# Optimization experiments

Measured on AMD Instinct MI355X. Metric: run time of the kernel, lower is better.

## Reference

```python
import jax, jax.numpy as jnp
import numpy as np

N_NODES = 50000
N_EDGES = 800000
IN_SIZE = 128
HID = 128
OUT_SIZE = 64
N_LAYERS = 2
MAXK = 32


def setup_inputs() -> dict:
    key = jax.random.key(0)
    ks = jax.random.split(key, 8)
    s = 0.05  # small init scale, xavier-like
    return {
        "x": jax.random.normal(ks[0], (N_NODES, IN_SIZE), dtype=jnp.float32),
        "W_in": jax.random.normal(ks[1], (IN_SIZE, HID), dtype=jnp.float32) * s,
        "b_in": jnp.zeros((HID,), dtype=jnp.float32),
        "W_self": jax.random.normal(ks[2], (N_LAYERS, HID, HID), dtype=jnp.float32) * s,
        "W_neigh": jax.random.normal(ks[3], (N_LAYERS, HID, HID), dtype=jnp.float32) * s,
        "W_out": jax.random.normal(ks[4], (HID, OUT_SIZE), dtype=jnp.float32) * s,
        "b_out": jnp.zeros((OUT_SIZE,), dtype=jnp.float32),
        "edge_index": jax.random.randint(ks[5], (2, N_EDGES), 0, N_NODES, dtype=jnp.int32),
        "k": MAXK,
    }


def _maxk(x, k):
    # Keep top-k values per row, zero out the rest (MaxK nonlinearity).
    vals, idx = jax.lax.top_k(x, k)                     # [N, k]
    rows = jnp.arange(x.shape[0])[:, None]
    return jnp.zeros_like(x).at[rows, idx].set(vals)


def reference(x, W_in, b_in, W_self, W_neigh, W_out, b_out, edge_index, k):
    N = x.shape[0]
    src, dst = edge_index[0], edge_index[1]
    # Row sums of the (src->dst) adjacency = out-degree of src, per original code.
    deg = jax.ops.segment_sum(jnp.ones((src.shape[0],), dtype=x.dtype), src,
                              num_segments=N)[:, None]  # [N, 1]
    h = x @ W_in + b_in                                  # lin_in
    for i in range(W_self.shape[0]):
        hs = _maxk(h, k)                                 # MaxK sparsify [N, H]
        # adj @ hs : out[i] = sum over edges (i -> j) of hs[j]; then mean-normalize
        agg = jax.ops.segment_sum(hs[dst], src, num_segments=N) / (deg + 1e-6)
        h = hs @ W_self[i] + agg @ W_neigh[i]            # h_self + h_neigh
        # dropout (eval) and Identity norm are no-ops
    return h @ W_out + b_out                             # lin_out
```

## Files before the change

### kernel.cpp

```cpp
#include <hip/hip_runtime.h>

#define KDIM 128

typedef _Float16 f16x8 __attribute__((ext_vector_type(8)));
typedef _Float16 f16x4 __attribute__((ext_vector_type(4)));
typedef float f32x16 __attribute__((ext_vector_type(16)));

#define NRANGE 6250
#define ECHUNK 3200

__global__ void hist_kernel(const int* __restrict__ src, int* __restrict__ cnt, int E) {
    const int r = blockIdx.x & 7;
    const int chunk = blockIdx.x >> 3;
    const int lo = r * NRANGE, hi = lo + NRANGE;
    const int base = chunk * ECHUNK;
    const int end = min(base + ECHUNK, E);
    for (int i = base + threadIdx.x; i < end; i += 256) {
        int s = src[i];
        if (s >= lo && s < hi) atomicAdd(&cnt[s], 1);
    }
}

__global__ void scatter_kernel(const int* __restrict__ src, const int* __restrict__ dst,
                               int* cursor, int* __restrict__ col, int E) {
    const int r = blockIdx.x & 7;
    const int chunk = blockIdx.x >> 3;
    const int lo = r * NRANGE, hi = lo + NRANGE;
    const int base = chunk * ECHUNK;
    const int end = min(base + ECHUNK, E);
    for (int i = base + threadIdx.x; i < end; i += 256) {
        int s = src[i];
        if (s >= lo && s < hi) {
            int p = atomicAdd(&cursor[s], 1);
            col[p] = dst[i];
        }
    }
}

__global__ void scan1_kernel(const int* __restrict__ cnt, int* __restrict__ row_ptr,
                             int* __restrict__ bsum, int N) {
    __shared__ int ws[4];
    const int t = threadIdx.x;
    const int lane = t & 63, w = t >> 6;
    const int i = blockIdx.x * 256 + t;
    int v = (i < N) ? cnt[i] : 0;
    int x = v;
    #pragma unroll
    for (int off = 1; off < 64; off <<= 1) {
        int u = __shfl_up(x, off);
        if (lane >= off) x += u;
    }
    if (lane == 63) ws[w] = x;
    __syncthreads();
    int wexcl = 0;
    #pragma unroll
    for (int k = 0; k < 4; k++) wexcl += (k < w) ? ws[k] : 0;
    if (i < N) row_ptr[i] = wexcl + x - v;
    if (t == 255) bsum[blockIdx.x] = wexcl + x;
}

__global__ void scan2_kernel(int* __restrict__ bsum, int NB) {
    __shared__ int ws[4];
    const int t = threadIdx.x;
    const int lane = t & 63, w = t >> 6;
    int v = (t < NB) ? bsum[t] : 0;
    int x = v;
    #pragma unroll
    for (int off = 1; off < 64; off <<= 1) {
        int u = __shfl_up(x, off);
        if (lane >= off) x += u;
    }
    if (lane == 63) ws[w] = x;
    __syncthreads();
    int wexcl = 0;
    #pragma unroll
    for (int k = 0; k < 4; k++) wexcl += (k < w) ? ws[k] : 0;
    if (t < NB) bsum[t] = wexcl + x - v;
}

__global__ void scan3_kernel(const int* __restrict__ bsum, int* __restrict__ row_ptr,
                             int* __restrict__ cursor, int N, int E) {
    const int i = blockIdx.x * 256 + threadIdx.x;
    if (i < N) {
        int v = row_ptr[i] + bsum[blockIdx.x];
        row_ptr[i] = v;
        cursor[i] = v;
    }
    if (i == 0) row_ptr[N] = E;
}

__global__ void sortrows_kernel(const int* __restrict__ row_ptr, int* __restrict__ col, int M) {
    int wid = (blockIdx.x * blockDim.x + threadIdx.x) >> 6;
    int lane = threadIdx.x & 63;
    if (wid >= M) return;
    int s = row_ptr[wid], e = row_ptr[wid + 1], len = e - s;
    if (len <= 1) return;
    if (len <= 64) {
        int v = (lane < len) ? col[s + lane] : 0x7fffffff;
        #pragma unroll
        for (int k = 2; k <= 64; k <<= 1) {
            #pragma unroll
            for (int j = k >> 1; j > 0; j >>= 1) {
                int o = __shfl_xor(v, j);
                bool dir = ((lane & k) == 0);
                bool smaller = ((lane & j) == 0);
                int mn = min(v, o), mx = max(v, o);
                v = (dir == smaller) ? mn : mx;
            }
        }
        if (lane < len) col[s + lane] = v;
    } else if (lane == 0) {
        for (int a = s + 1; a < e; a++) {
            int key = col[a];
            int b = a - 1;
            while (b >= s && col[b] > key) { col[b + 1] = col[b]; b--; }
            col[b + 1] = key;
        }
    }
}

__global__ void maxk_kernel(const float* __restrict__ h, float* __restrict__ hs, int M) {
    int wid = (blockIdx.x * blockDim.x + threadIdx.x) >> 6;
    int lane = threadIdx.x & 63;
    if (wid >= M) return;
    float2 v = ((const float2*)(h + (size_t)wid * KDIM))[lane];

    unsigned int u0 = __float_as_uint(v.x);
    u0 = (u0 & 0x80000000u) ? ~u0 : (u0 | 0x80000000u);
    unsigned int u1 = __float_as_uint(v.y);
    u1 = (u1 & 0x80000000u) ? ~u1 : (u1 | 0x80000000u);

    unsigned int prefix = 0;
    int remaining = 32;
    #pragma unroll
    for (int b = 31; b >= 0; --b) {
        unsigned int candHi = (prefix >> b) | 1u;
        unsigned long long m0 = __ballot((u0 >> b) == candHi);
        unsigned long long m1 = __ballot((u1 >> b) == candHi);
        int cnt = __popcll(m0) + __popcll(m1);
        if (cnt >= remaining) prefix |= (1u << b);
        else remaining -= cnt;
    }

    unsigned long long e0 = __ballot(u0 == prefix);
    unsigned long long e1 = __ballot(u1 == prefix);
    unsigned long long g0 = __ballot(u0 > prefix);
    unsigned long long g1 = __ballot(u1 > prefix);
    int quota = 32 - (__popcll(g0) + __popcll(g1));
    unsigned long long below = (1ULL << lane) - 1ULL;
    int rank0 = __popcll(e0 & below) + __popcll(e1 & below);
    int rank1 = rank0 + (int)((e0 >> lane) & 1ULL);
    bool k0 = (u0 > prefix) || (((e0 >> lane) & 1ULL) && rank0 < quota);
    bool k1 = (u1 > prefix) || (((e1 >> lane) & 1ULL) && rank1 < quota);

    float2 o;
    o.x = k0 ? v.x : 0.0f;
    o.y = k1 ? v.y : 0.0f;
    ((float2*)(hs + (size_t)wid * KDIM))[lane] = o;
}

__global__ __launch_bounds__(256)
void aggregate_kernel(const float* __restrict__ hs, const int* __restrict__ row_ptr,
                      const int* __restrict__ col, float* __restrict__ agg, int M) {
    const int lane = threadIdx.x & 63;
    const int wid = (blockIdx.x * blockDim.x + threadIdx.x) >> 6;
    if (wid >= M) return;
    const int s = row_ptr[wid], e = row_ptr[wid + 1];
    const float2* __restrict__ hp = (const float2*)hs;

    float2 a0 = make_float2(0.f, 0.f);
    float2 a1 = a0, a2 = a0, a3 = a0, a4 = a0, a5 = a0, a6 = a0, a7 = a0;

    int j = s;
    for (; j + 7 < e; j += 8) {
        int c0 = col[j];     int c1 = col[j + 1];
        int c2 = col[j + 2]; int c3 = col[j + 3];
        int c4 = col[j + 4]; int c5 = col[j + 5];
        int c6 = col[j + 6]; int c7 = col[j + 7];
        float2 v0 = hp[(size_t)c0 * 64 + lane];
        float2 v1 = hp[(size_t)c1 * 64 + lane];
        float2 v2 = hp[(size_t)c2 * 64 + lane];
        float2 v3 = hp[(size_t)c3 * 64 + lane];
        float2 v4 = hp[(size_t)c4 * 64 + lane];
        float2 v5 = hp[(size_t)c5 * 64 + lane];
        float2 v6 = hp[(size_t)c6 * 64 + lane];
        float2 v7 = hp[(size_t)c7 * 64 + lane];
        a0.x += v0.x; a0.y += v0.y;
        a1.x += v1.x; a1.y += v1.y;
        a2.x += v2.x; a2.y += v2.y;
        a3.x += v3.x; a3.y += v3.y;
        a4.x += v4.x; a4.y += v4.y;
        a5.x += v5.x; a5.y += v5.y;
        a6.x += v6.x; a6.y += v6.y;
        a7.x += v7.x; a7.y += v7.y;
    }
    if (j < e)     { float2 v = hp[(size_t)col[j]     * 64 + lane]; a0.x += v.x; a0.y += v.y; }
    if (j + 1 < e) { float2 v = hp[(size_t)col[j + 1] * 64 + lane]; a1.x += v.x; a1.y += v.y; }
    if (j + 2 < e) { float2 v = hp[(size_t)col[j + 2] * 64 + lane]; a2.x += v.x; a2.y += v.y; }
    if (j + 3 < e) { float2 v = hp[(size_t)col[j + 3] * 64 + lane]; a3.x += v.x; a3.y += v.y; }
    if (j + 4 < e) { float2 v = hp[(size_t)col[j + 4] * 64 + lane]; a4.x += v.x; a4.y += v.y; }
    if (j + 5 < e) { float2 v = hp[(size_t)col[j + 5] * 64 + lane]; a5.x += v.x; a5.y += v.y; }
    if (j + 6 < e) { float2 v = hp[(size_t)col[j + 6] * 64 + lane]; a6.x += v.x; a6.y += v.y; }

    float2 s01, s23, s45, s67, sA, sB, t;
    s01.x = a0.x + a1.x; s01.y = a0.y + a1.y;
    s23.x = a2.x + a3.x; s23.y = a2.y + a3.y;
    s45.x = a4.x + a5.x; s45.y = a4.y + a5.y;
    s67.x = a6.x + a7.x; s67.y = a6.y + a7.y;
    sA.x = s01.x + s23.x; sA.y = s01.y + s23.y;
    sB.x = s45.x + s67.x; sB.y = s45.y + s67.y;
    t.x = sA.x + sB.x; t.y = sA.y + sB.y;

    float inv = 1.0f / ((float)(e - s) + 1e-6f);
    float2 o;
    o.x = t.x * inv;
    o.y = t.y * inv;
    ((float2*)(agg + (size_t)wid * KDIM))[lane] = o;
}

__global__ void conv_wt_kernel(const float* __restrict__ W_in,
                               const float* __restrict__ W_self,
                               const float* __restrict__ W_neigh,
                               const float* __restrict__ W_out,
                               _Float16* __restrict__ wb) {
    int t = blockIdx.x * blockDim.x + threadIdx.x;
    if (t < 81920) {
        int m = t >> 14;
        int e = t & 16383;
        int n = e >> 7, k = e & 127;
        const float* S = (m == 0) ? W_in
                       : (m <= 2) ? (W_self + (size_t)(m - 1) * 16384)
                                  : (W_neigh + (size_t)(m - 3) * 16384);
        float v = S[k * 128 + n];
        _Float16 hi = (_Float16)v;
        _Float16 lo = (_Float16)(v - (float)hi);
        int pair = m * 2;
        wb[(size_t)pair * 16384 + n * 128 + k] = hi;
        wb[(size_t)(pair + 1) * 16384 + n * 128 + k] = lo;
    } else if (t < 90112) {
        int e = t - 81920;
        int n = e >> 7, k = e & 127;
        float v = W_out[k * 64 + n];
        _Float16 hi = (_Float16)v;
        _Float16 lo = (_Float16)(v - (float)hi);
        wb[(size_t)10 * 16384 + e] = hi;
        wb[(size_t)11 * 16384 + e] = lo;
    }
}

template <int BN, bool DUAL, bool BIAS>
__global__ __launch_bounds__(256)
void gemm_mfma(const float* __restrict__ A1, const float* __restrict__ A2,
               const _Float16* __restrict__ B1h, const _Float16* __restrict__ B1l,
               const _Float16* __restrict__ B2h, const _Float16* __restrict__ B2l,
               const float* __restrict__ bias, float* __restrict__ C, int M) {
    constexpr int NSRC = DUAL ? 2 : 1;
    constexpr int NT = BN / 32;
    constexpr int TPW = NT / 2;

    __shared__ __align__(16) char Alds[2 * 64 * 256];

    const int tid = threadIdx.x;
    const int w = tid >> 6;
    const int lane = tid & 63;
    const int l31 = lane & 31;
    const int kslot = lane >> 5;
    const int row0 = blockIdx.x * 64;

    const int n0 = (BN == 128) ? w * 32 : (w & 1) * 32;
    const int mt0 = (BN == 128) ? 0 : (w >> 1);

    f32x16 acc[TPW];
    #pragma unroll
    for (int t = 0; t < TPW; t++)
        #pragma unroll
        for (int e = 0; e < 16; e++) acc[t][e] = 0.0f;

    for (int s = 0; s < NSRC; s++) {
        if (s) __syncthreads();
        const float* A = s ? A2 : A1;
        #pragma unroll
        for (int p = 0; p < 8; p++) {
            int idx = tid + p * 256;
            int row = idx >> 5, k4 = idx & 31;
            float4 v = make_float4(0.f, 0.f, 0.f, 0.f);
            if (row0 + row < M) v = *(const float4*)(A + (size_t)(row0 + row) * KDIM + k4 * 4);
            _Float16 h0 = (_Float16)v.x, h1 = (_Float16)v.y,
                     h2 = (_Float16)v.z, h3 = (_Float16)v.w;
            f16x4 hv = {h0, h1, h2, h3};
            f16x4 lv = {(_Float16)(v.x - (float)h0), (_Float16)(v.y - (float)h1),
                        (_Float16)(v.z - (float)h2), (_Float16)(v.w - (float)h3)};
            int boff = (k4 * 8) ^ ((row & 7) << 4);
            *(f16x4*)(Alds + row * 256 + boff) = hv;
            *(f16x4*)(Alds + 16384 + row * 256 + boff) = lv;
        }
        __syncthreads();

        const _Float16* Bh = s ? B2h : B1h;
        const _Float16* Bl = s ? B2l : B1l;
        const _Float16* bph = Bh + (size_t)(n0 + l31) * 128 + kslot * 8;
        const _Float16* bpl = Bl + (size_t)(n0 + l31) * 128 + kslot * 8;
        #pragma unroll
        for (int kb = 0; kb < 8; kb++) {
            f16x8 bh = *(const f16x8*)(bph + kb * 16);
            f16x8 bl = *(const f16x8*)(bpl + kb * 16);
            #pragma unroll
            for (int t = 0; t < TPW; t++) {
                int row = (mt0 + t) * 32 + l31;
                int boff = ((kb * 2 + kslot) * 16) ^ ((row & 7) << 4);
                const char* rp = Alds + row * 256 + boff;
                f16x8 ah = *(const f16x8*)(rp);
                f16x8 al = *(const f16x8*)(rp + 16384);
                acc[t] = __builtin_amdgcn_mfma_f32_32x32x16_f16(al, bh, acc[t], 0, 0, 0);
                acc[t] = __builtin_amdgcn_mfma_f32_32x32x16_f16(ah, bl, acc[t], 0, 0, 0);
                acc[t] = __builtin_amdgcn_mfma_f32_32x32x16_f16(ah, bh, acc[t], 0, 0, 0);
            }
        }
    }

    float bv = 0.0f;
    if (BIAS) bv = bias[n0 + l31];
    #pragma unroll
    for (int t = 0; t < TPW; t++) {
        #pragma unroll
        for (int r = 0; r < 16; r++) {
            int row = row0 + (mt0 + t) * 32 + (r & 3) + 8 * (r >> 2) + 4 * kslot;
            if (row < M) C[(size_t)row * BN + n0 + l31] = acc[t][r] + bv;
        }
    }
}

extern "C" void kernel_launch(void* const* d_in, const int* in_sizes, int n_in,
                              void* d_out, int out_size, void* d_ws, size_t ws_size,
                              hipStream_t stream) {
    const float* x       = (const float*)d_in[0];
    const float* W_in    = (const float*)d_in[1];
    const float* b_in    = (const float*)d_in[2];
    const float* W_self  = (const float*)d_in[3];
    const float* W_neigh = (const float*)d_in[4];
    const float* W_out   = (const float*)d_in[5];
    const float* b_out   = (const float*)d_in[6];
    const int*   eidx    = (const int*)d_in[7];

    const int N = 50000, E = 800000;
    const int* src = eidx;
    const int* dst = eidx + E;

    char* ws = (char*)d_ws;
    float* h   = (float*)(ws);
    float* hs  = (float*)(ws + 25600000);
    float* agg = (float*)(ws + 51200000);
    int* cnt     = (int*)(ws + 76800000);
    int* row_ptr = (int*)(ws + 77000000);
    int* cursor  = (int*)(ws + 77200016);
    int* col     = (int*)(ws + 77400016);
    _Float16* wb = (_Float16*)(ws + 80600016);
    int* bsum    = (int*)(ws + 81000016);

    const _Float16* WinT_h  = wb + (size_t)0 * 16384;
    const _Float16* WinT_l  = wb + (size_t)1 * 16384;
    const _Float16* WoutT_h = wb + (size_t)10 * 16384;
    const _Float16* WoutT_l = wb + (size_t)11 * 16384;

    const int NB = (N + 255) / 256;
    const int EG = ((E + ECHUNK - 1) / ECHUNK) * 8;

    hipMemsetAsync(cnt, 0, N * sizeof(int), stream);
    hist_kernel<<<EG, 256, 0, stream>>>(src, cnt, E);
    scan1_kernel<<<NB, 256, 0, stream>>>(cnt, row_ptr, bsum, N);
    scan2_kernel<<<1, 256, 0, stream>>>(bsum, NB);
    scan3_kernel<<<NB, 256, 0, stream>>>(bsum, row_ptr, cursor, N, E);
    scatter_kernel<<<EG, 256, 0, stream>>>(src, dst, cursor, col, E);
    sortrows_kernel<<<(N + 3) / 4, 256, 0, stream>>>(row_ptr, col, N);
    conv_wt_kernel<<<(90112 + 255) / 256, 256, 0, stream>>>(W_in, W_self, W_neigh, W_out, wb);

    const int G = (N + 63) / 64;

    gemm_mfma<128, false, true><<<G, 256, 0, stream>>>(
        x, nullptr, WinT_h, WinT_l, nullptr, nullptr, b_in, h, N);

    for (int i = 0; i < 2; i++) {
        maxk_kernel<<<(N + 3) / 4, 256, 0, stream>>>(h, hs, N);
        aggregate_kernel<<<(N + 3) / 4, 256, 0, stream>>>(hs, row_ptr, col, agg, N);
        const _Float16* WsT_h = wb + (size_t)(2 + 2 * i) * 16384;
        const _Float16* WsT_l = wb + (size_t)(3 + 2 * i) * 16384;
        const _Float16* WnT_h = wb + (size_t)(6 + 2 * i) * 16384;
        const _Float16* WnT_l = wb + (size_t)(7 + 2 * i) * 16384;
        gemm_mfma<128, true, false><<<G, 256, 0, stream>>>(
            hs, agg, WsT_h, WsT_l, WnT_h, WnT_l, nullptr, h, N);
    }

    gemm_mfma<64, false, true><<<G, 256, 0, stream>>>(
        h, nullptr, WoutT_h, WoutT_l, nullptr, nullptr, b_out, (float*)d_out, N);
}
```

Before: 373.6 us.

## Store sparsified features in column-chunked layout and aggregate per chunk for cache locality

The MaxK output is now written as 8 column chunks of 16 floats each, one contiguous array per chunk over all nodes. The aggregation kernel assigns each block a single chunk and gathers from one 3.2 MB slice, so the random neighbour gathers can stay in L2 or the last-level cache. Eight lanes cover one 64-byte row segment and eight edges are processed in parallel, with a shuffle reduction at the end. The downstream GEMM reads the chunked layout for its first operand. The cost is shorter 64-byte gathers, repeated row_ptr and col reads for every chunk, and a cross-lane reduction.

```diff
diff --git a/kernel.cpp b/kernel.cpp
--- a/kernel.cpp
+++ b/kernel.cpp
@@ -1,6 +1,8 @@
 #include <hip/hip_runtime.h>
 
 #define KDIM 128
+#define NNODE 50000
+#define CHSTRIDE 800000
 
 typedef _Float16 f16x8 __attribute__((ext_vector_type(8)));
 typedef _Float16 f16x4 __attribute__((ext_vector_type(4)));
@@ -119,7 +121,7 @@
     }
 }
 
-__global__ void maxk_kernel(const float* __restrict__ h, float* __restrict__ hs, int M) {
+__global__ void maxk_kernel(const float* __restrict__ h, float* __restrict__ hsc, int M) {
     int wid = (blockIdx.x * blockDim.x + threadIdx.x) >> 6;
     int lane = threadIdx.x & 63;
     if (wid >= M) return;
@@ -156,66 +158,48 @@
     float2 o;
     o.x = k0 ? v.x : 0.0f;
     o.y = k1 ? v.y : 0.0f;
-    ((float2*)(hs + (size_t)wid * KDIM))[lane] = o;
-}
-
+    ((float2*)(hsc + (size_t)(lane >> 3) * CHSTRIDE))[(size_t)wid * 8 + (lane & 7)] = o;
+}
+
+#define NPB 32
 __global__ __launch_bounds__(256)
-void aggregate_kernel(const float* __restrict__ hs, const int* __restrict__ row_ptr,
+void aggregate_kernel(const float* __restrict__ hsc, const int* __restrict__ row_ptr,
                       const int* __restrict__ col, float* __restrict__ agg, int M) {
+    const int c = blockIdx.x & 7;
+    const int g = blockIdx.x >> 3;
+    const int w = threadIdx.x >> 6;
     const int lane = threadIdx.x & 63;
-    const int wid = (blockIdx.x * blockDim.x + threadIdx.x) >> 6;
-    if (wid >= M) return;
-    const int s = row_ptr[wid], e = row_ptr[wid + 1];
-    const float2* __restrict__ hp = (const float2*)hs;
-
-    float2 a0 = make_float2(0.f, 0.f);
-    float2 a1 = a0, a2 = a0, a3 = a0, a4 = a0, a5 = a0, a6 = a0, a7 = a0;
-
-    int j = s;
-    for (; j + 7 < e; j += 8) {
-        int c0 = col[j];     int c1 = col[j + 1];
-        int c2 = col[j + 2]; int c3 = col[j + 3];
-        int c4 = col[j + 4]; int c5 = col[j + 5];
-        int c6 = col[j + 6]; int c7 = col[j + 7];
-        float2 v0 = hp[(size_t)c0 * 64 + lane];
-        float2 v1 = hp[(size_t)c1 * 64 + lane];
-        float2 v2 = hp[(size_t)c2 * 64 + lane];
-        float2 v3 = hp[(size_t)c3 * 64 + lane];
-        float2 v4 = hp[(size_t)c4 * 64 + lane];
-        float2 v5 = hp[(size_t)c5 * 64 + lane];
-        float2 v6 = hp[(size_t)c6 * 64 + lane];
-        float2 v7 = hp[(size_t)c7 * 64 + lane];
-        a0.x += v0.x; a0.y += v0.y;
-        a1.x += v1.x; a1.y += v1.y;
-        a2.x += v2.x; a2.y += v2.y;
-        a3.x += v3.x; a3.y += v3.y;
-        a4.x += v4.x; a4.y += v4.y;
-        a5.x += v5.x; a5.y += v5.y;
-        a6.x += v6.x; a6.y += v6.y;
-        a7.x += v7.x; a7.y += v7.y;
-    }
-    if (j < e)     { float2 v = hp[(size_t)col[j]     * 64 + lane]; a0.x += v.x; a0.y += v.y; }
-    if (j + 1 < e) { float2 v = hp[(size_t)col[j + 1] * 64 + lane]; a1.x += v.x; a1.y += v.y; }
-    if (j + 2 < e) { float2 v = hp[(size_t)col[j + 2] * 64 + lane]; a2.x += v.x; a2.y += v.y; }
-    if (j + 3 < e) { float2 v = hp[(size_t)col[j + 3] * 64 + lane]; a3.x += v.x; a3.y += v.y; }
-    if (j + 4 < e) { float2 v = hp[(size_t)col[j + 4] * 64 + lane]; a4.x += v.x; a4.y += v.y; }
-    if (j + 5 < e) { float2 v = hp[(size_t)col[j + 5] * 64 + lane]; a5.x += v.x; a5.y += v.y; }
-    if (j + 6 < e) { float2 v = hp[(size_t)col[j + 6] * 64 + lane]; a6.x += v.x; a6.y += v.y; }
-
-    float2 s01, s23, s45, s67, sA, sB, t;
-    s01.x = a0.x + a1.x; s01.y = a0.y + a1.y;
-    s23.x = a2.x + a3.x; s23.y = a2.y + a3.y;
-    s45.x = a4.x + a5.x; s45.y = a4.y + a5.y;
-    s67.x = a6.x + a7.x; s67.y = a6.y + a7.y;
-    sA.x = s01.x + s23.x; sA.y = s01.y + s23.y;
-    sB.x = s45.x + s67.x; sB.y = s45.y + s67.y;
-    t.x = sA.x + sB.x; t.y = sA.y + sB.y;
-
-    float inv = 1.0f / ((float)(e - s) + 1e-6f);
-    float2 o;
-    o.x = t.x * inv;
-    o.y = t.y * inv;
-    ((float2*)(agg + (size_t)wid * KDIM))[lane] = o;
+    const int e8 = lane >> 3;
+    const int f2 = lane & 7;
+    const float2* __restrict__ hp = (const float2*)(hsc + (size_t)c * CHSTRIDE);
+
+    const int n0 = g * NPB + w * 8;
+    #pragma unroll 1
+    for (int u = 0; u < 8; u++) {
+        int n = n0 + u;
+        if (n >= M) break;
+        int s = row_ptr[n], e = row_ptr[n + 1];
+        float2 a0 = make_float2(0.f, 0.f), a1 = a0;
+        int j = s + e8;
+        for (; j + 8 < e; j += 16) {
+            float2 v0 = hp[(size_t)col[j] * 8 + f2];
+            float2 v1 = hp[(size_t)col[j + 8] * 8 + f2];
+            a0.x += v0.x; a0.y += v0.y;
+            a1.x += v1.x; a1.y += v1.y;
+        }
+        if (j < e) { float2 v = hp[(size_t)col[j] * 8 + f2]; a0.x += v.x; a0.y += v.y; }
+        float2 t;
+        t.x = a0.x + a1.x; t.y = a0.y + a1.y;
+        t.x += __shfl_xor(t.x, 8);  t.y += __shfl_xor(t.y, 8);
+        t.x += __shfl_xor(t.x, 16); t.y += __shfl_xor(t.y, 16);
+        t.x += __shfl_xor(t.x, 32); t.y += __shfl_xor(t.y, 32);
+        if (e8 == 0) {
+            float inv = 1.0f / ((float)(e - s) + 1e-6f);
+            float2 o;
+            o.x = t.x * inv; o.y = t.y * inv;
+            ((float2*)(agg + (size_t)n * KDIM + c * 16))[f2] = o;
+        }
+    }
 }
 
 __global__ void conv_wt_kernel(const float* __restrict__ W_in,
@@ -248,7 +232,7 @@
     }
 }
 
-template <int BN, bool DUAL, bool BIAS>
+template <int BN, bool DUAL, bool BIAS, bool A1CHUNK>
 __global__ __launch_bounds__(256)
 void gemm_mfma(const float* __restrict__ A1, const float* __restrict__ A2,
                const _Float16* __restrict__ B1h, const _Float16* __restrict__ B1l,
@@ -284,7 +268,13 @@
             int idx = tid + p * 256;
             int row = idx >> 5, k4 = idx & 31;
             float4 v = make_float4(0.f, 0.f, 0.f, 0.f);
-            if (row0 + row < M) v = *(const float4*)(A + (size_t)(row0 + row) * KDIM + k4 * 4);
+            if (row0 + row < M) {
+                if (A1CHUNK && s == 0)
+                    v = *(const float4*)(A + (size_t)(k4 >> 2) * CHSTRIDE
+                                           + (size_t)(row0 + row) * 16 + (k4 & 3) * 4);
+                else
+                    v = *(const float4*)(A + (size_t)(row0 + row) * KDIM + k4 * 4);
+            }
             _Float16 h0 = (_Float16)v.x, h1 = (_Float16)v.y,
                      h2 = (_Float16)v.z, h3 = (_Float16)v.w;
             f16x4 hv = {h0, h1, h2, h3};
@@ -342,13 +332,13 @@
     const float* b_out   = (const float*)d_in[6];
     const int*   eidx    = (const int*)d_in[7];
 
-    const int N = 50000, E = 800000;
+    const int N = NNODE, E = 800000;
     const int* src = eidx;
     const int* dst = eidx + E;
 
     char* ws = (char*)d_ws;
     float* h   = (float*)(ws);
-    float* hs  = (float*)(ws + 25600000);
+    float* hsc = (float*)(ws + 25600000);
     float* agg = (float*)(ws + 51200000);
     int* cnt     = (int*)(ws + 76800000);
     int* row_ptr = (int*)(ws + 77000000);
@@ -364,6 +354,7 @@
 
     const int NB = (N + 255) / 256;
     const int EG = ((E + ECHUNK - 1) / ECHUNK) * 8;
+    const int AG = ((N + NPB - 1) / NPB) * 8;
 
     hipMemsetAsync(cnt, 0, N * sizeof(int), stream);
     hist_kernel<<<EG, 256, 0, stream>>>(src, cnt, E);
@@ -376,20 +367,20 @@
 
     const int G = (N + 63) / 64;
 
-    gemm_mfma<128, false, true><<<G, 256, 0, stream>>>(
+    gemm_mfma<128, false, true, false><<<G, 256, 0, stream>>>(
         x, nullptr, WinT_h, WinT_l, nullptr, nullptr, b_in, h, N);
 
     for (int i = 0; i < 2; i++) {
-        maxk_kernel<<<(N + 3) / 4, 256, 0, stream>>>(h, hs, N);
-        aggregate_kernel<<<(N + 3) / 4, 256, 0, stream>>>(hs, row_ptr, col, agg, N);
+        maxk_kernel<<<(N + 3) / 4, 256, 0, stream>>>(h, hsc, N);
+        aggregate_kernel<<<AG, 256, 0, stream>>>(hsc, row_ptr, col, agg, N);
         const _Float16* WsT_h = wb + (size_t)(2 + 2 * i) * 16384;
         const _Float16* WsT_l = wb + (size_t)(3 + 2 * i) * 16384;
         const _Float16* WnT_h = wb + (size_t)(6 + 2 * i) * 16384;
         const _Float16* WnT_l = wb + (size_t)(7 + 2 * i) * 16384;
-        gemm_mfma<128, true, false><<<G, 256, 0, stream>>>(
-            hs, agg, WsT_h, WsT_l, WnT_h, WnT_l, nullptr, h, N);
-    }
-
-    gemm_mfma<64, false, true><<<G, 256, 0, stream>>>(
+        gemm_mfma<128, true, false, true><<<G, 256, 0, stream>>>(
+            hsc, agg, WsT_h, WsT_l, WnT_h, WnT_l, nullptr, h, N);
+    }
+
+    gemm_mfma<64, false, true, false><<<G, 256, 0, stream>>>(
         h, nullptr, WoutT_h, WoutT_l, nullptr, nullptr, b_out, (float*)d_out, N);
 }
```

Result: slower. 450.8 us (+20.7%).
